# Kernel tuning notes

Measured on AMD Instinct MI355X. Metric: run time of the kernel, lower is better.

Reference implementation:

```python
import jax, jax.numpy as jnp
import numpy as np

D = 1024  # decoder_hidden_dim


def setup_inputs() -> dict:
    key = jax.random.key(0)
    k1, k2, k3, k4 = jax.random.split(key, 4)
    b, s, d = 32, 2048, D
    decoder_hidden = jax.random.normal(k1, (b, d), dtype=jnp.float32)
    encoder_all_hidden = jax.random.normal(k2, (b, s, d), dtype=jnp.float32)
    # torch nn.Linear(2d, d, bias=False): weight shape (d, 2d)
    W_a = jax.random.normal(k3, (d, 2 * d), dtype=jnp.float32) * (1.0 / np.sqrt(2 * d))
    # torch nn.Linear(d, 1, bias=False): weight shape (1, d) -> store as (d,)
    v = jax.random.normal(k4, (d,), dtype=jnp.float32) * (1.0 / np.sqrt(d))
    return {"decoder_hidden": decoder_hidden, "encoder_all_hidden": encoder_all_hidden,
            "W_a": W_a, "v": v}


def reference(decoder_hidden, encoder_all_hidden, W_a, v):
    d = W_a.shape[0]
    # Split W_a so the (b, s, 2d) concat is never materialized:
    # cat([dec, enc]) @ W_a^T == dec @ Wd^T + enc @ We^T
    Wd = W_a[:, :d]   # acts on decoder part
    We = W_a[:, d:]   # acts on encoder part
    dec_proj = jnp.einsum('bd,ed->be', decoder_hidden, Wd)          # (b, d)
    enc_proj = jnp.einsum('bsd,ed->bse', encoder_all_hidden, We)    # (b, s, d)
    h = jnp.tanh(dec_proj[:, None, :] + enc_proj)                   # (b, s, d)
    scores = jnp.einsum('bse,e->bs', h, v)                          # (b, s)
    alpha = jax.nn.softmax(scores, axis=1)
    return alpha
```

## Files before the change

### kernel.cpp

```cpp
#include <hip/hip_runtime.h>
#include <hip/hip_bf16.h>
#include <stdint.h>


typedef __bf16 bf16x8 __attribute__((ext_vector_type(8)));
typedef __bf16 bf16x2 __attribute__((ext_vector_type(2)));
typedef float floatx4 __attribute__((ext_vector_type(4)));

#define M_TOT 65536
#define D_DIM 1024
#define WA_LD 2048
#define S_DIM 2048

__device__ __forceinline__ unsigned int pack2(float a, float b) {
#if __has_builtin(__builtin_amdgcn_cvt_pk_bf16_f32)
    bf16x2 p = __builtin_amdgcn_cvt_pk_bf16_f32(a, b);
    return __builtin_bit_cast(unsigned int, p);
#else
    unsigned int ua = __float_as_uint(a), ub = __float_as_uint(b);
    ua += 0x7fffu + ((ua >> 16) & 1u);
    ub += 0x7fffu + ((ub >> 16) & 1u);
    return __builtin_amdgcn_perm(ub, ua, 0x07060302);
#endif
}

__global__ __launch_bounds__(256) void decproj_kernel(
    const float* __restrict__ dec,
    const float* __restrict__ Wa,
    float* __restrict__ dp)
{
    const int b    = blockIdx.y;
    const int wave = threadIdx.x >> 6;
    const int lane = threadIdx.x & 63;
    const int e    = blockIdx.x * 4 + wave;

    __shared__ float s_d[1024];
    for (int t = threadIdx.x; t < 1024; t += 256)
        s_d[t] = dec[b * 1024 + t];
    __syncthreads();

    const float* wrow = Wa + (size_t)e * WA_LD;
    float sum = 0.f;
    #pragma unroll
    for (int k0 = 0; k0 < 1024; k0 += 256) {
        float4 w = *(const float4*)(wrow + k0 + lane * 4);
        float4 d = *(const float4*)(&s_d[k0 + lane * 4]);
        sum += w.x * d.x + w.y * d.y + w.z * d.z + w.w * d.w;
    }
    #pragma unroll
    for (int msk = 1; msk < 64; msk <<= 1)
        sum += __shfl_xor(sum, msk, 64);
    if (lane == 0)
        dp[b * 1024 + e] = sum;
}

__global__ __launch_bounds__(256) void fused_gemm_kernel(
    const float* __restrict__ enc,
    const float* __restrict__ Wa,
    const float* __restrict__ v,
    const float* __restrict__ dp,
    float* __restrict__ partial)
{
    __shared__ unsigned short As[128 * 32];
    __shared__ unsigned short Bs[128 * 32];
    __shared__ float s_dec[128];
    __shared__ float s_v[128];
    __shared__ float s_score[128];

    const int tid  = threadIdx.x;
    const int lane = tid & 63;
    const int wave = tid >> 6;
    const int wm   = wave >> 1;
    const int wn   = wave & 1;

    const int flat    = blockIdx.y * 8 + blockIdx.x;
    const int n_block = (flat >> 3) & 7;
    const int m_block = (flat & 7) | ((flat >> 6) << 3);
    const int b_idx   = m_block >> 4;

    if (tid < 128) {
        s_dec[tid] = dp[b_idx * 1024 + n_block * 128 + tid];
        s_v[tid]   = v[n_block * 128 + tid];
    }

    const int r0  = tid >> 2;
    const int kk  = (tid & 3) * 8;
    const int r16 = lane & 15;
    const int q   = lane >> 4;

    const float* A_base = enc + (size_t)m_block * 128 * D_DIM;
    const float* B_base = Wa + (size_t)n_block * 128 * WA_LD + D_DIM;

    floatx4 acc[4][4] = {};

    for (int k0 = 0; k0 < 1024; k0 += 32) {
        float4 a0l = *(const float4*)(A_base + (size_t)r0        * D_DIM + k0 + kk);
        float4 a0h = *(const float4*)(A_base + (size_t)r0        * D_DIM + k0 + kk + 4);
        float4 a1l = *(const float4*)(A_base + (size_t)(r0 + 64) * D_DIM + k0 + kk);
        float4 a1h = *(const float4*)(A_base + (size_t)(r0 + 64) * D_DIM + k0 + kk + 4);
        float4 b0l = *(const float4*)(B_base + (size_t)r0        * WA_LD + k0 + kk);
        float4 b0h = *(const float4*)(B_base + (size_t)r0        * WA_LD + k0 + kk + 4);
        float4 b1l = *(const float4*)(B_base + (size_t)(r0 + 64) * WA_LD + k0 + kk);
        float4 b1h = *(const float4*)(B_base + (size_t)(r0 + 64) * WA_LD + k0 + kk + 4);
        uint4 pa0 = { pack2(a0l.x, a0l.y), pack2(a0l.z, a0l.w), pack2(a0h.x, a0h.y), pack2(a0h.z, a0h.w) };
        uint4 pa1 = { pack2(a1l.x, a1l.y), pack2(a1l.z, a1l.w), pack2(a1h.x, a1h.y), pack2(a1h.z, a1h.w) };
        uint4 pb0 = { pack2(b0l.x, b0l.y), pack2(b0l.z, b0l.w), pack2(b0h.x, b0h.y), pack2(b0h.z, b0h.w) };
        uint4 pb1 = { pack2(b1l.x, b1l.y), pack2(b1l.z, b1l.w), pack2(b1h.x, b1h.y), pack2(b1h.z, b1h.w) };
        __syncthreads();
        *(uint4*)&As[r0        * 32 + kk] = pa0;
        *(uint4*)&As[(r0 + 64) * 32 + kk] = pa1;
        *(uint4*)&Bs[r0        * 32 + kk] = pb0;
        *(uint4*)&Bs[(r0 + 64) * 32 + kk] = pb1;
        __syncthreads();

        bf16x8 af[4], bfr[4];
        #pragma unroll
        for (int i = 0; i < 4; ++i)
            af[i] = *(const bf16x8*)&As[(wm * 64 + i * 16 + r16) * 32 + q * 8];
        #pragma unroll
        for (int j = 0; j < 4; ++j)
            bfr[j] = *(const bf16x8*)&Bs[(wn * 64 + j * 16 + r16) * 32 + q * 8];
        #pragma unroll
        for (int i = 0; i < 4; ++i)
            #pragma unroll
            for (int j = 0; j < 4; ++j)
                acc[i][j] = __builtin_amdgcn_mfma_f32_16x16x32_bf16(af[i], bfr[j], acc[i][j], 0, 0, 0);
    }

    float p[4][4] = {};
    #pragma unroll
    for (int j = 0; j < 4; ++j) {
        const int nl = wn * 64 + j * 16 + r16;
        const float dd = s_dec[nl];
        const float vv = s_v[nl];
        #pragma unroll
        for (int i = 0; i < 4; ++i) {
            #pragma unroll
            for (int r = 0; r < 4; ++r) {
                float x = acc[i][j][r] + dd;
                if (!(x > -8.f)) x = -8.f;
                if (x > 8.f)     x = 8.f;
                float e2 = __expf(2.f * x);
                float h  = 1.f - 2.f * __builtin_amdgcn_rcpf(e2 + 1.f);
                p[i][r] += h * vv;
            }
        }
    }
    #pragma unroll
    for (int msk = 1; msk < 16; msk <<= 1) {
        #pragma unroll
        for (int i = 0; i < 4; ++i)
            #pragma unroll
            for (int r = 0; r < 4; ++r)
                p[i][r] += __shfl_xor(p[i][r], msk, 64);
    }
    __syncthreads();
    if (wn == 0 && r16 == 0) {
        #pragma unroll
        for (int i = 0; i < 4; ++i)
            #pragma unroll
            for (int r = 0; r < 4; ++r)
                s_score[wm * 64 + i * 16 + q * 4 + r] = p[i][r];
    }
    __syncthreads();
    if (wn == 1 && r16 == 0) {
        #pragma unroll
        for (int i = 0; i < 4; ++i)
            #pragma unroll
            for (int r = 0; r < 4; ++r)
                s_score[wm * 64 + i * 16 + q * 4 + r] += p[i][r];
    }
    __syncthreads();
    if (tid < 128)
        partial[(size_t)n_block * M_TOT + m_block * 128 + tid] = s_score[tid];
}

__global__ __launch_bounds__(256) void softmax_kernel(
    const float* __restrict__ partial,
    float* __restrict__ out)
{
    const int b = blockIdx.x;
    const int tid = threadIdx.x;
    __shared__ float wmax[4], wsum[4];

    float sc[8];
    float mx = -1e30f;
    #pragma unroll
    for (int ii = 0; ii < 8; ++ii) {
        const int s = tid + ii * 256;
        float sum = 0.f;
        #pragma unroll
        for (int pp = 0; pp < 8; ++pp)
            sum += partial[(size_t)pp * M_TOT + b * S_DIM + s];
        sc[ii] = sum;
        mx = fmaxf(mx, sum);
    }
    #pragma unroll
    for (int msk = 1; msk < 64; msk <<= 1) mx = fmaxf(mx, __shfl_xor(mx, msk, 64));
    if ((tid & 63) == 0) wmax[tid >> 6] = mx;
    __syncthreads();
    mx = fmaxf(fmaxf(wmax[0], wmax[1]), fmaxf(wmax[2], wmax[3]));

    float ex[8];
    float tot = 0.f;
    #pragma unroll
    for (int ii = 0; ii < 8; ++ii) { ex[ii] = __expf(sc[ii] - mx); tot += ex[ii]; }
    #pragma unroll
    for (int msk = 1; msk < 64; msk <<= 1) tot += __shfl_xor(tot, msk, 64);
    if ((tid & 63) == 0) wsum[tid >> 6] = tot;
    __syncthreads();
    tot = wsum[0] + wsum[1] + wsum[2] + wsum[3];
    const float inv = 1.f / tot;
    #pragma unroll
    for (int ii = 0; ii < 8; ++ii)
        out[b * S_DIM + tid + ii * 256] = ex[ii] * inv;
}

extern "C" void kernel_launch(void* const* d_in, const int* in_sizes, int n_in,
                              void* d_out, int out_size, void* d_ws, size_t ws_size,
                              hipStream_t stream) {
    (void)in_sizes; (void)n_in; (void)out_size; (void)ws_size;
    const float* dec = (const float*)d_in[0];
    const float* enc = (const float*)d_in[1];
    const float* Wa  = (const float*)d_in[2];
    const float* v   = (const float*)d_in[3];
    float* out = (float*)d_out;

    float* dp      = (float*)d_ws;
    float* partial = dp + 32 * 1024;

    decproj_kernel<<<dim3(256, 32), 256, 0, stream>>>(dec, Wa, dp);
    fused_gemm_kernel<<<dim3(8, 512), 256, 0, stream>>>(enc, Wa, v, dp, partial);
    softmax_kernel<<<32, 256, 0, stream>>>(partial, out);
}
```

Measured before the change: 591.5 us.

## Pre-convert encoder and weights to bf16 and load tiles via global_load_lds

Adds two pre-pass kernels that convert the encoder activations and the encoder half of W_a to bf16 in workspace. A new GEMM kernel then streams bf16 tiles straight into a swizzled LDS layout with global_load_lds, instead of loading fp32, packing in registers and storing to LDS on every k-step. This cuts per-tile global traffic and VALU conversion work inside the GEMM loop. The cost is an extra full read of the fp32 encoder plus a bf16 write and re-read, and the new path only runs when the workspace is large enough.

Measured after the change: 569.6 us. 1.04x faster.

```diff
diff --git a/kernel.cpp b/kernel.cpp
--- a/kernel.cpp
+++ b/kernel.cpp
@@ -6,6 +6,7 @@
 typedef __bf16 bf16x8 __attribute__((ext_vector_type(8)));
 typedef __bf16 bf16x2 __attribute__((ext_vector_type(2)));
 typedef float floatx4 __attribute__((ext_vector_type(4)));
+typedef unsigned short ushort_t;
 
 #define M_TOT 65536
 #define D_DIM 1024
@@ -24,6 +25,36 @@
 #endif
 }
 
+__device__ __forceinline__ void gl16(const ushort_t* g, ushort_t* l) {
+    __builtin_amdgcn_global_load_lds(
+        (const __attribute__((address_space(1))) unsigned int*)g,
+        (__attribute__((address_space(3))) unsigned int*)l,
+        16, 0, 0);
+}
+
+__global__ __launch_bounds__(256) void convertW_kernel(
+    const float* __restrict__ Wa, ushort_t* __restrict__ Web)
+{
+    const int e = blockIdx.x;
+    const int k = threadIdx.x * 4;
+    float4 wv = *(const float4*)(Wa + (size_t)e * WA_LD + D_DIM + k);
+    uint2 pk = { pack2(wv.x, wv.y), pack2(wv.z, wv.w) };
+    *(uint2*)(Web + (size_t)e * D_DIM + k) = pk;
+}
+
+__global__ __launch_bounds__(256) void convert_enc_kernel(
+    const float* __restrict__ in, ushort_t* __restrict__ out)
+{
+    size_t i = ((size_t)blockIdx.x * 256 + threadIdx.x) * 8;
+    const size_t stride = (size_t)4096 * 256 * 8;
+    for (int it = 0; it < 8; ++it, i += stride) {
+        float4 a = *(const float4*)(in + i);
+        float4 b = *(const float4*)(in + i + 4);
+        uint4 pk = { pack2(a.x, a.y), pack2(a.z, a.w), pack2(b.x, b.y), pack2(b.z, b.w) };
+        *(uint4*)(out + i) = pk;
+    }
+}
+
 __global__ __launch_bounds__(256) void decproj_kernel(
     const float* __restrict__ dec,
     const float* __restrict__ Wa,
@@ -54,7 +85,127 @@
         dp[b * 1024 + e] = sum;
 }
 
-__global__ __launch_bounds__(256) void fused_gemm_kernel(
+__global__ __launch_bounds__(256) void gemm_bf16_kernel(
+    const ushort_t* __restrict__ A,
+    const ushort_t* __restrict__ Bw,
+    const float* __restrict__ v,
+    const float* __restrict__ dp,
+    float* __restrict__ partial)
+{
+    __shared__ ushort_t As[128 * 32];
+    __shared__ ushort_t Bs[128 * 32];
+    __shared__ float s_dec[128], s_v[128], s_score[128];
+
+    const int tid  = threadIdx.x;
+    const int lane = tid & 63;
+    const int w    = tid >> 6;
+    const int wm   = w >> 1;
+    const int wn   = w & 1;
+    const int r16  = lane & 15;
+    const int q    = lane >> 4;
+
+    const int flat    = blockIdx.y * 8 + blockIdx.x;
+    const int n_block = (flat >> 3) & 7;
+    const int m_block = (flat & 7) | ((flat >> 6) << 3);
+    const int b_idx   = m_block >> 4;
+
+    if (tid < 128) {
+        s_dec[tid] = dp[b_idx * 1024 + n_block * 128 + tid];
+        s_v[tid]   = v[n_block * 128 + tid];
+    }
+
+    const int sr = (w << 4) + (lane >> 2);
+    const int fS = (sr & 3) ^ ((sr >> 2) & 1);
+    const int sg = ((lane & 3) ^ fS) << 3;
+    const ushort_t* Ag = A  + (size_t)(m_block * 128 + sr) * D_DIM + sg;
+    const ushort_t* Bg = Bw + (size_t)(n_block * 128 + sr) * D_DIM + sg;
+    ushort_t* AsW0 = &As[(w << 4) * 32];
+    ushort_t* AsW1 = &As[(64 + (w << 4)) * 32];
+    ushort_t* BsW0 = &Bs[(w << 4) * 32];
+    ushort_t* BsW1 = &Bs[(64 + (w << 4)) * 32];
+
+    const int fR = (r16 & 3) ^ ((r16 >> 2) & 1);
+    const int sl = (q ^ fR) << 3;
+    const ushort_t* pa[4];
+    const ushort_t* pb[4];
+    #pragma unroll
+    for (int i = 0; i < 4; ++i) {
+        pa[i] = &As[(wm * 64 + i * 16 + r16) * 32 + sl];
+        pb[i] = &Bs[(wn * 64 + i * 16 + r16) * 32 + sl];
+    }
+
+    floatx4 acc[4][4] = {};
+
+    for (int t = 0; t < 32; ++t) {
+        const int k0 = t * 32;
+        __syncthreads();
+        gl16(Ag + k0,              AsW0);
+        gl16(Ag + k0 + 64 * D_DIM, AsW1);
+        gl16(Bg + k0,              BsW0);
+        gl16(Bg + k0 + 64 * D_DIM, BsW1);
+        __syncthreads();
+
+        bf16x8 af[4], bfr[4];
+        #pragma unroll
+        for (int i = 0; i < 4; ++i) af[i]  = *(const bf16x8*)pa[i];
+        #pragma unroll
+        for (int j = 0; j < 4; ++j) bfr[j] = *(const bf16x8*)pb[j];
+        #pragma unroll
+        for (int i = 0; i < 4; ++i)
+            #pragma unroll
+            for (int j = 0; j < 4; ++j)
+                acc[i][j] = __builtin_amdgcn_mfma_f32_16x16x32_bf16(af[i], bfr[j], acc[i][j], 0, 0, 0);
+    }
+
+    float p[4][4] = {};
+    #pragma unroll
+    for (int j = 0; j < 4; ++j) {
+        const int nl = wn * 64 + j * 16 + r16;
+        const float dd = s_dec[nl];
+        const float vv = s_v[nl];
+        #pragma unroll
+        for (int i = 0; i < 4; ++i) {
+            #pragma unroll
+            for (int r = 0; r < 4; ++r) {
+                float x = acc[i][j][r] + dd;
+                if (!(x > -8.f)) x = -8.f;
+                if (x > 8.f)     x = 8.f;
+                float e2 = __expf(2.f * x);
+                float h  = 1.f - 2.f * __builtin_amdgcn_rcpf(e2 + 1.f);
+                p[i][r] += h * vv;
+            }
+        }
+    }
+    #pragma unroll
+    for (int msk = 1; msk < 16; msk <<= 1) {
+        #pragma unroll
+        for (int i = 0; i < 4; ++i)
+            #pragma unroll
+            for (int r = 0; r < 4; ++r)
+                p[i][r] += __shfl_xor(p[i][r], msk, 64);
+    }
+    __syncthreads();
+    if (wn == 0 && r16 == 0) {
+        #pragma unroll
+        for (int i = 0; i < 4; ++i)
+            #pragma unroll
+            for (int r = 0; r < 4; ++r)
+                s_score[wm * 64 + i * 16 + q * 4 + r] = p[i][r];
+    }
+    __syncthreads();
+    if (wn == 1 && r16 == 0) {
+        #pragma unroll
+        for (int i = 0; i < 4; ++i)
+            #pragma unroll
+            for (int r = 0; r < 4; ++r)
+                s_score[wm * 64 + i * 16 + q * 4 + r] += p[i][r];
+    }
+    __syncthreads();
+    if (tid < 128)
+        partial[(size_t)n_block * M_TOT + m_block * 128 + tid] = s_score[tid];
+}
+
+__global__ __launch_bounds__(256) void fused_gemm_fp32_kernel(
     const float* __restrict__ enc,
     const float* __restrict__ Wa,
     const float* __restrict__ v,
@@ -219,7 +370,7 @@
 extern "C" void kernel_launch(void* const* d_in, const int* in_sizes, int n_in,
                               void* d_out, int out_size, void* d_ws, size_t ws_size,
                               hipStream_t stream) {
-    (void)in_sizes; (void)n_in; (void)out_size; (void)ws_size;
+    (void)in_sizes; (void)n_in; (void)out_size;
     const float* dec = (const float*)d_in[0];
     const float* enc = (const float*)d_in[1];
     const float* Wa  = (const float*)d_in[2];
@@ -229,7 +380,20 @@
     float* dp      = (float*)d_ws;
     float* partial = dp + 32 * 1024;
 
-    decproj_kernel<<<dim3(256, 32), 256, 0, stream>>>(dec, Wa, dp);
-    fused_gemm_kernel<<<dim3(8, 512), 256, 0, stream>>>(enc, Wa, v, dp, partial);
+    const size_t NEED = (size_t)(32 * 1024 + 8 * 65536) * 4
+                      + (size_t)67108864 * 2
+                      + (size_t)1048576 * 2;
+
+    if (ws_size >= NEED) {
+        ushort_t* encb = (ushort_t*)(partial + 8 * 65536);
+        ushort_t* Web  = encb + 67108864;
+        convertW_kernel<<<dim3(1024), 256, 0, stream>>>(Wa, Web);
+        convert_enc_kernel<<<dim3(4096), 256, 0, stream>>>(enc, encb);
+        decproj_kernel<<<dim3(256, 32), 256, 0, stream>>>(dec, Wa, dp);
+        gemm_bf16_kernel<<<dim3(8, 512), 256, 0, stream>>>(encb, Web, v, dp, partial);
+    } else {
+        decproj_kernel<<<dim3(256, 32), 256, 0, stream>>>(dec, Wa, dp);
+        fused_gemm_fp32_kernel<<<dim3(8, 512), 256, 0, stream>>>(enc, Wa, v, dp, partial);
+    }
     softmax_kernel<<<32, 256, 0, stream>>>(partial, out);
 }
```
